# Kernel optimization log

Measured on AMD Instinct MI355X. Metric: run time of the kernel, lower is better.

The kernel has to match this reference:

```python
import jax, jax.numpy as jnp
import numpy as np

B, N1, N2, D, H = 2, 1024, 1024, 2048, 16
DH = D // H  # 128


def _rope_tables(S, d):
    inv = 1.0 / (10000.0 ** (np.arange(0, d, 2, dtype=np.float32) / d))
    ang = np.outer(np.arange(S, dtype=np.float32), inv)  # [S, d/2]
    cos = np.repeat(np.cos(ang), 2, axis=-1).astype(np.float32)  # [S, d] interleaved pairs
    sin = np.repeat(np.sin(ang), 2, axis=-1).astype(np.float32)
    return jnp.asarray(cos), jnp.asarray(sin)


def setup_inputs() -> dict:
    key = jax.random.key(0)
    ks = jax.random.split(key, 24)
    sc = 0.02
    cos1, sin1 = _rope_tables(N1, DH)
    cos2, sin2 = _rope_tables(N2, DH)
    inp = {
        'x_1': jax.random.normal(ks[0], (B, N1, D), dtype=jnp.float32),
        'x_2': jax.random.normal(ks[1], (B, N2, D), dtype=jnp.float32),
        'cos1': cos1, 'sin1': sin1, 'cos2': cos2, 'sin2': sin2,
    }
    names = ['wq1', 'wk1', 'wv1', 'wo1', 'wq2', 'wk2', 'wv2', 'wo2']
    for i, n in enumerate(names):
        inp[n] = jax.random.normal(ks[2 + i], (D, D), dtype=jnp.float32) * sc
        inp['b' + n[1:]] = jax.random.normal(ks[10 + i], (D,), dtype=jnp.float32) * sc
    return inp


def _apply_rope(x, cos, sin):
    # x: [B, H, S, DH]; interleaved-pair rotation (use_real_unbind_dim=-1)
    xr = x.reshape(*x.shape[:-1], -1, 2)
    x_real, x_imag = xr[..., 0], xr[..., 1]
    x_rot = jnp.stack([-x_imag, x_real], axis=-1).reshape(x.shape)
    return x * cos[None, None] + x_rot * sin[None, None]


def _split_heads(t):
    b, n, _ = t.shape
    return t.reshape(b, n, H, DH).transpose(0, 2, 1, 3)  # b h n c


def reference(x_1, x_2, cos1, sin1, cos2, sin2,
              wq1, bq1, wk1, bk1, wv1, bv1, wo1, bo1,
              wq2, bq2, wk2, bk2, wv2, bv2, wo2, bo2):
    len_1 = x_1.shape[1]
    q = jnp.concatenate([x_1 @ wq1 + bq1, x_2 @ wq2 + bq2], axis=1)
    k = jnp.concatenate([x_1 @ wk1 + bk1, x_2 @ wk2 + bk2], axis=1)
    v = jnp.concatenate([x_1 @ wv1 + bv1, x_2 @ wv2 + bv2], axis=1)
    q, k, v = _split_heads(q), _split_heads(k), _split_heads(v)
    q = q * (DH ** -0.5)
    # per-position RoPE on the concatenated stream == per-stream RoPE then concat
    cos = jnp.concatenate([cos1, cos2], axis=0)
    sin = jnp.concatenate([sin1, sin2], axis=0)
    q = _apply_rope(q, cos, sin)
    k = _apply_rope(k, cos, sin)
    # joint attention over both streams (independent/cross_only flags = False)
    scores = jnp.einsum('bhqd,bhkd->bhqk', q, k)
    attn = jax.nn.softmax(scores, axis=-1)
    o = jnp.einsum('bhqk,bhkd->bhqd', attn, v)
    o = o.transpose(0, 2, 1, 3).reshape(o.shape[0], -1, H * DH)  # b n (h c)
    o1 = o[:, :len_1] @ wo1 + bo1
    o2 = o[:, len_1:] @ wo2 + bo2
    return (o1, o2)
```

## Files before the change

kernel.cpp:

```cpp
#include <hip/hip_runtime.h>
#include <hip/hip_bf16.h>

typedef __attribute__((ext_vector_type(4))) float f32x4;
typedef __attribute__((ext_vector_type(8))) short short8;
typedef __attribute__((ext_vector_type(4))) unsigned short us4;
typedef __attribute__((ext_vector_type(2))) unsigned short us2;
typedef unsigned short u16;

__device__ __forceinline__ float bf2f(u16 u) {
  unsigned int x = ((unsigned int)u) << 16;
  float f; __builtin_memcpy(&f, &x, 4); return f;
}
__device__ __forceinline__ u16 f2bf(float f) {
  __hip_bfloat16 h = __float2bfloat16(f);
  u16 u; __builtin_memcpy(&u, &h, 2); return u;
}

#define GLL16(g, l) __builtin_amdgcn_global_load_lds( \
    (const __attribute__((address_space(1))) unsigned int*)(g), \
    (__attribute__((address_space(3))) unsigned int*)(l), 16, 0, 0)

#define MFMA16x32(a, b, c) __builtin_amdgcn_mfma_f32_16x16x32_bf16(a, b, c, 0, 0, 0)


__global__ __launch_bounds__(256) void k_convert_x(const float* __restrict__ x1,
                                                   const float* __restrict__ x2,
                                                   u16* __restrict__ xc) {
  int tid = blockIdx.x * 256 + threadIdx.x;
  int e = tid * 8;
  int m = e >> 11, d = e & 2047;
  int b = m >> 11, n = m & 2047;
  const float* src = (n < 1024) ? (x1 + ((b << 10) + n) * 2048 + d)
                                : (x2 + ((b << 10) + n - 1024) * 2048 + d);
  float4 v0 = *(const float4*)src;
  float4 v1 = *(const float4*)(src + 4);
  us4 a = {f2bf(v0.x), f2bf(v0.y), f2bf(v0.z), f2bf(v0.w)};
  us4 c = {f2bf(v1.x), f2bf(v1.y), f2bf(v1.z), f2bf(v1.w)};
  *(us4*)(xc + e) = a;
  *(us4*)(xc + e + 4) = c;
}

struct W8 { const float* w[8]; };

__global__ __launch_bounds__(256) void k_wt(W8 p, u16* __restrict__ wtbase) {
  __shared__ u16 lt[64][72];
  const float* W = p.w[blockIdx.z];
  u16* Wt = wtbase + (size_t)blockIdx.z * 4194304u;
  int k0 = blockIdx.x * 64, n0 = blockIdx.y * 64;
  int t = threadIdx.x;
#pragma unroll
  for (int i = 0; i < 4; ++i) {
    int lin = t + i * 256;
    int r = lin >> 4, c4 = (lin & 15) * 4;
    float4 v = *(const float4*)&W[(k0 + r) * 2048 + n0 + c4];
    us4 u = {f2bf(v.x), f2bf(v.y), f2bf(v.z), f2bf(v.w)};
    *(us4*)&lt[r][c4] = u;
  }
  __syncthreads();
#pragma unroll
  for (int i = 0; i < 8; ++i) {
    int lin = t + i * 256;
    int rd = lin >> 5, cs = (lin & 31) * 2;
    us2 u = {lt[cs][rd], lt[cs + 1][rd]};
    *(us2*)&Wt[(n0 + rd) * 2048 + k0 + cs] = u;
  }
}

__global__ __launch_bounds__(256) void k_vt(const u16* __restrict__ V, u16* __restrict__ Vt) {
  __shared__ u16 lt[64][72];
  int b = blockIdx.z;
  int s0 = blockIdx.x * 64, d0 = blockIdx.y * 64;
  int t = threadIdx.x;
#pragma unroll
  for (int i = 0; i < 2; ++i) {
    int lin = t + i * 256;
    int r = lin >> 3, c8 = (lin & 7) * 8;
    short8 v = *(const short8*)&V[(b * 2048 + s0 + r) * 2048 + d0 + c8];
    *(short8*)&lt[r][c8] = v;
  }
  __syncthreads();
#pragma unroll
  for (int i = 0; i < 8; ++i) {
    int lin = t + i * 256;
    int rd = lin >> 5, cs = (lin & 31) * 2;
    us2 u = {lt[cs][rd], lt[cs + 1][rd]};
    *(us2*)&Vt[(b * 2048 + d0 + rd) * 2048 + s0 + cs] = u;
  }
}

__global__ __launch_bounds__(256) void k_rope(u16* __restrict__ Qb, u16* __restrict__ Kb,
                                              const float* __restrict__ cos1,
                                              const float* __restrict__ sin1,
                                              const float* __restrict__ cos2,
                                              const float* __restrict__ sin2) {
  u16* T = blockIdx.y ? Kb : Qb;
  const float scale = blockIdx.y ? 1.f : 0.08838834764831843f;
  int tid = blockIdx.x * 256 + threadIdx.x;
  int e = tid * 8;
  int m = e >> 11;
  int n = m & 2047;
  int dh0 = e & 127;
  const float* cr; const float* sr;
  if (n < 1024) { cr = cos1 + n * 128; sr = sin1 + n * 128; }
  else          { cr = cos2 + (n - 1024) * 128; sr = sin2 + (n - 1024) * 128; }
  float4 c0 = *(const float4*)(cr + dh0), c1 = *(const float4*)(cr + dh0 + 4);
  float4 s0 = *(const float4*)(sr + dh0), s1 = *(const float4*)(sr + dh0 + 4);
  short8 xv = *(short8*)(T + e);
  float x0 = bf2f((u16)xv[0]), x1 = bf2f((u16)xv[1]), x2 = bf2f((u16)xv[2]), x3 = bf2f((u16)xv[3]);
  float x4 = bf2f((u16)xv[4]), x5 = bf2f((u16)xv[5]), x6 = bf2f((u16)xv[6]), x7 = bf2f((u16)xv[7]);
  us4 o0 = { f2bf((x0 * c0.x - x1 * s0.x) * scale), f2bf((x1 * c0.x + x0 * s0.x) * scale),
             f2bf((x2 * c0.z - x3 * s0.z) * scale), f2bf((x3 * c0.z + x2 * s0.z) * scale) };
  us4 o1 = { f2bf((x4 * c1.x - x5 * s1.x) * scale), f2bf((x5 * c1.x + x4 * s1.x) * scale),
             f2bf((x6 * c1.z - x7 * s1.z) * scale), f2bf((x7 * c1.z + x6 * s1.z) * scale) };
  *(us4*)(T + e) = o0;
  *(us4*)(T + e + 4) = o1;
}

__device__ __forceinline__ void gemm256_core(const u16* __restrict__ A,
                                             const u16* __restrict__ Bt,
                                             int m0, int nb,
                                             u16* lA, u16* lB,
                                             f32x4 acc[8][4]) {
  const int t = threadIdx.x;
  const int lane = t & 63, wid = t >> 6;
  const int lq = lane & 15, lg = lane >> 4;
  const int wr = wid >> 2, wc = wid & 3;
  const int swz = (lq & 7) << 4;

  u16* lA0 = lA;  u16* lA1 = lA + 256 * 64;
  u16* lB0 = lB;  u16* lB1 = lB + 256 * 64;

  short8 af[4][2];
  short8 bf[2][2][2];

  auto stage = [&](const u16* G, int grow0, u16* lbase, int h, int kt) {
    const int k0 = (kt & 31) * 64;
#pragma unroll
    for (int j = 0; j < 2; ++j) {
      int c = j * 512 + t;
      int row = c >> 3;
      int colb = (c & 7) * 16;
      int sc = colb ^ ((row & 7) << 4);
      GLL16(G + (size_t)(grow0 + h * 128 + row) * 2048 + k0 + (sc >> 1),
            (u16*)((char*)lbase + (h * 128 + row) * 128 + colb));
    }
  };
  auto rdA = [&](const u16* lbase, int mh) {
#pragma unroll
    for (int mf = 0; mf < 4; ++mf)
#pragma unroll
      for (int kc = 0; kc < 2; ++kc) {
        int row = wr * 128 + (mh * 4 + mf) * 16 + lq;
        af[mf][kc] = *(const short8*)((const char*)lbase + row * 128 +
                                      ((kc * 64 + lg * 16) ^ swz));
      }
  };
  auto rdB = [&](const u16* lbase, int nh) {
#pragma unroll
    for (int nf = 0; nf < 2; ++nf)
#pragma unroll
      for (int kc = 0; kc < 2; ++kc) {
        int row = wc * 64 + (nh * 2 + nf) * 16 + lq;
        bf[nh][nf][kc] = *(const short8*)((const char*)lbase + row * 128 +
                                          ((kc * 64 + lg * 16) ^ swz));
      }
  };
  auto mm = [&](int mh, int nh) {
    __builtin_amdgcn_s_setprio(1);
#pragma unroll
    for (int mf = 0; mf < 4; ++mf)
#pragma unroll
      for (int nf = 0; nf < 2; ++nf)
#pragma unroll
        for (int kc = 0; kc < 2; ++kc)
          acc[mh * 4 + mf][nh * 2 + nf] =
              MFMA16x32(af[mf][kc], bf[nh][nf][kc], acc[mh * 4 + mf][nh * 2 + nf]);
    __builtin_amdgcn_s_setprio(0);
    __builtin_amdgcn_sched_barrier(0);
  };

#define LGK0() do { asm volatile("s_waitcnt lgkmcnt(0)" ::: "memory"); \
                    __builtin_amdgcn_sched_barrier(0); } while (0)
#define BAR()  __builtin_amdgcn_s_barrier()
#define VM4()  asm volatile("s_waitcnt vmcnt(4)" ::: "memory")

  stage(Bt, nb, lB0, 0, 0);
  stage(A,  m0, lA0, 0, 0);
  stage(Bt, nb, lB0, 1, 0);
  stage(A,  m0, lA0, 1, 0);
  stage(Bt, nb, lB1, 0, 1);
  stage(A,  m0, lA1, 0, 1);
  VM4();
  BAR();

#pragma unroll 1
  for (int i = 0; i < 16; ++i) {
    const int o1 = 2 * i + 1, e2 = 2 * i + 2, o3 = 2 * i + 3;
    rdA(lA0, 0); rdB(lB0, 0);
    stage(Bt, nb, lB1, 1, o1);
    BAR(); LGK0(); mm(0, 0); BAR();
    rdB(lB0, 1);
    stage(A, m0, lA1, 1, o1);
    BAR(); LGK0(); mm(0, 1); BAR();
    rdA(lA0, 1);
    stage(Bt, nb, lB0, 0, e2);
    BAR(); LGK0(); mm(1, 0); BAR();
    stage(A, m0, lA0, 0, e2);
    BAR(); LGK0(); mm(1, 1);
    VM4(); BAR();
    rdA(lA1, 0); rdB(lB1, 0);
    stage(Bt, nb, lB0, 1, e2);
    BAR(); LGK0(); mm(0, 0); BAR();
    rdB(lB1, 1);
    stage(A, m0, lA0, 1, e2);
    BAR(); LGK0(); mm(0, 1); BAR();
    rdA(lA1, 1);
    stage(Bt, nb, lB1, 0, o3);
    BAR(); LGK0(); mm(1, 0); BAR();
    stage(A, m0, lA1, 0, o3);
    BAR(); LGK0(); mm(1, 1);
    VM4(); BAR();
  }
#undef LGK0
#undef BAR
#undef VM4
}

struct QKV8P {
  const u16* wt[6];
  const float* bias[6];
  u16* out[3];
  const u16* xc;
};

__global__ __launch_bounds__(512, 2) void k_gemm_qkv(QKV8P p) {
  __shared__ __align__(16) u16 lA[2 * 256 * 64];
  __shared__ __align__(16) u16 lB[2 * 256 * 64];
  const int id = blockIdx.x;
  const int xcd = id & 7, sub = id >> 3;
  const int nt = xcd * 3 + (sub >> 4);
  const int mt = sub & 15;
  const int m0 = mt * 256;
  const int type = nt >> 3;
  const int colw = (nt & 7) * 256;
  const int strm = (mt >> 2) & 1;
  const int widx = type * 2 + strm;
  f32x4 acc[8][4];
  const f32x4 z4 = {0.f, 0.f, 0.f, 0.f};
#pragma unroll
  for (int a = 0; a < 8; ++a)
#pragma unroll
    for (int b = 0; b < 4; ++b) acc[a][b] = z4;
  gemm256_core(p.xc, p.wt[widx], m0, colw, lA, lB, acc);
  const int lane = threadIdx.x & 63, wid = threadIdx.x >> 6;
  const int lq = lane & 15, lg = lane >> 4;
  const int wr = wid >> 2, wc = wid & 3;
  u16* out = p.out[type];
  const float* bias = p.bias[widx];
#pragma unroll
  for (int nf = 0; nf < 4; ++nf) {
    int col = colw + wc * 64 + nf * 16 + lq;
    float bv = bias[col];
#pragma unroll
    for (int mf = 0; mf < 8; ++mf) {
      int row0 = m0 + wr * 128 + mf * 16 + lg * 4;
#pragma unroll
      for (int j = 0; j < 4; ++j)
        out[(size_t)(row0 + j) * 2048 + col] = f2bf(acc[mf][nf][j] + bv);
    }
  }
}

__global__ __launch_bounds__(512, 2) void k_gemm_out(const u16* __restrict__ O,
                                                     const u16* __restrict__ wt0,
                                                     const u16* __restrict__ wt1,
                                                     const float* __restrict__ b0,
                                                     const float* __restrict__ b1,
                                                     float* __restrict__ out) {
  __shared__ __align__(16) u16 lA[2 * 256 * 64];
  __shared__ __align__(16) u16 lB[2 * 256 * 64];
  const int id = blockIdx.x;
  const int nt = id & 7, mt = id >> 3;
  const int m0 = mt * 256;
  const int strm = (mt >> 2) & 1;
  f32x4 acc[8][4];
  const f32x4 z4 = {0.f, 0.f, 0.f, 0.f};
#pragma unroll
  for (int a = 0; a < 8; ++a)
#pragma unroll
    for (int b = 0; b < 4; ++b) acc[a][b] = z4;
  gemm256_core(O, strm ? wt1 : wt0, m0, nt * 256, lA, lB, acc);
  const float* bias = strm ? b1 : b0;
  float* obase = strm ? out + 4194304 : out;
  const int lane = threadIdx.x & 63, wid = threadIdx.x >> 6;
  const int lq = lane & 15, lg = lane >> 4;
  const int wr = wid >> 2, wc = wid & 3;
#pragma unroll
  for (int nf = 0; nf < 4; ++nf) {
    int col = nt * 256 + wc * 64 + nf * 16 + lq;
    float bv = bias[col];
#pragma unroll
    for (int mf = 0; mf < 8; ++mf) {
      int row0 = m0 + wr * 128 + mf * 16 + lg * 4;
#pragma unroll
      for (int j = 0; j < 4; ++j) {
        int row = row0 + j;
        int b = row >> 11, n = row & 2047;
        obase[(size_t)(b * 1024 + n - strm * 1024) * 2048 + col] = acc[mf][nf][j] + bv;
      }
    }
  }
}

__global__ __launch_bounds__(256) void k_attn(const u16* __restrict__ Q,
                                              const u16* __restrict__ K,
                                              const u16* __restrict__ Vt,
                                              u16* __restrict__ O) {
  __shared__ __align__(16) u16 kbuf[2][64 * 128];
  __shared__ __align__(16) u16 vbuf[2][128 * 64];
  __shared__ __align__(16) u16 pbuf[4][16 * 88];
  const int t = threadIdx.x, lane = t & 63, w = t >> 6;
  const int lq = lane & 15, g = lane >> 4;
  const int id = blockIdx.x;
  const int lgid = (id & 7) * 64 + (id >> 3);
  const int bh = lgid >> 4, qt = lgid & 15;
  const int b = bh >> 4, h = bh & 15;

  short8 qf[2][4];
#pragma unroll
  for (int u = 0; u < 2; ++u) {
    const u16* Qp = Q + (size_t)(b * 2048 + qt * 128 + w * 32 + u * 16 + lq) * 2048
                    + h * 128 + g * 8;
#pragma unroll
    for (int c = 0; c < 4; ++c) qf[u][c] = *(const short8*)(Qp + c * 32);
  }

  f32x4 oacc[2][8];
  const f32x4 z4 = {0.f, 0.f, 0.f, 0.f};
#pragma unroll
  for (int u = 0; u < 2; ++u)
#pragma unroll
    for (int dc = 0; dc < 8; ++dc) oacc[u][dc] = z4;
  float m_run[2] = {-1e30f, -1e30f}, l_run[2] = {0.f, 0.f};

  const int swz = (lq & 7) << 4;

  auto STAGE = [&](int bs, int kt) {
#pragma unroll
    for (int ii = 0; ii < 4; ++ii) {
      int i = w * 4 + ii;
      int o = i * 1024 + lane * 16;
      {
        int row = o >> 8, colb = o & 255;
        int sc = colb ^ ((row & 7) << 4);
        GLL16(K + (size_t)(b * 2048 + kt + row) * 2048 + h * 128 + (sc >> 1),
              (u16*)((char*)kbuf[bs] + o));
      }
      {
        int row = o >> 7, colb = o & 127;
        int sc = colb ^ ((row & 7) << 4);
        GLL16(Vt + (size_t)(b * 2048 + h * 128 + row) * 2048 + kt + (sc >> 1),
              (u16*)((char*)vbuf[bs] + o));
      }
    }
  };

  STAGE(0, 0);
  asm volatile("s_waitcnt vmcnt(0)" ::: "memory");
  __syncthreads();

  for (int tt = 0; tt < 32; ++tt) {
    const int cb = tt & 1;
    if (tt < 31) STAGE(cb ^ 1, (tt + 1) * 64);

    const char* kb = (const char*)kbuf[cb];
    const char* vb = (const char*)vbuf[cb];
    f32x4 s[2][4];
#pragma unroll
    for (int u = 0; u < 2; ++u)
#pragma unroll
      for (int kg = 0; kg < 4; ++kg) s[u][kg] = z4;
#pragma unroll
    for (int c = 0; c < 4; ++c) {
#pragma unroll
      for (int kg = 0; kg < 4; ++kg) {
        short8 kf = *(const short8*)(kb + (kg * 16 + lq) * 256 + ((c * 64 + g * 16) ^ swz));
        s[0][kg] = MFMA16x32(kf, qf[0][c], s[0][kg]);
        s[1][kg] = MFMA16x32(kf, qf[1][c], s[1][kg]);
      }
    }
    u16* pw = pbuf[w];
    short8 pb[2][2];
#pragma unroll
    for (int u = 0; u < 2; ++u) {
      float pm = -1e30f;
#pragma unroll
      for (int kg = 0; kg < 4; ++kg)
#pragma unroll
        for (int j = 0; j < 4; ++j) pm = fmaxf(pm, s[u][kg][j]);
      pm = fmaxf(pm, __shfl_xor(pm, 16));
      pm = fmaxf(pm, __shfl_xor(pm, 32));
      const float mnew = fmaxf(m_run[u], pm);
      const float r = __expf(m_run[u] - mnew);
      m_run[u] = mnew;
      float ps = 0.f;
#pragma unroll
      for (int kg = 0; kg < 4; ++kg) {
        float p0 = __expf(s[u][kg][0] - mnew), p1 = __expf(s[u][kg][1] - mnew);
        float p2 = __expf(s[u][kg][2] - mnew), p3 = __expf(s[u][kg][3] - mnew);
        ps += (p0 + p1) + (p2 + p3);
        us4 wv = {f2bf(p0), f2bf(p1), f2bf(p2), f2bf(p3)};
        *(us4*)(pw + lq * 88 + kg * 16 + g * 4) = wv;
      }
      ps += __shfl_xor(ps, 16);
      ps += __shfl_xor(ps, 32);
      l_run[u] = l_run[u] * r + ps;
#pragma unroll
      for (int dc = 0; dc < 8; ++dc) oacc[u][dc] = oacc[u][dc] * r;
      pb[u][0] = *(const short8*)(pw + lq * 88 + g * 8);
      pb[u][1] = *(const short8*)(pw + lq * 88 + 32 + g * 8);
    }
#pragma unroll
    for (int kc = 0; kc < 2; ++kc) {
#pragma unroll
      for (int dc = 0; dc < 8; ++dc) {
        short8 vf = *(const short8*)(vb + (dc * 16 + lq) * 128 + ((kc * 64 + g * 16) ^ swz));
        oacc[0][dc] = MFMA16x32(vf, pb[0][kc], oacc[0][dc]);
        oacc[1][dc] = MFMA16x32(vf, pb[1][kc], oacc[1][dc]);
      }
    }
    asm volatile("s_waitcnt vmcnt(0)" ::: "memory");
    __syncthreads();
  }

#pragma unroll
  for (int u = 0; u < 2; ++u) {
    const float inv = 1.f / l_run[u];
    u16* Op = O + (size_t)(b * 2048 + qt * 128 + w * 32 + u * 16 + lq) * 2048
              + h * 128 + g * 4;
#pragma unroll
    for (int dc = 0; dc < 8; ++dc) {
      us4 ov = {f2bf(oacc[u][dc][0] * inv), f2bf(oacc[u][dc][1] * inv),
                f2bf(oacc[u][dc][2] * inv), f2bf(oacc[u][dc][3] * inv)};
      *(us4*)(Op + dc * 16) = ov;
    }
  }
}


extern "C" void kernel_launch(void* const* d_in, const int* in_sizes, int n_in,
                              void* d_out, int out_size, void* d_ws, size_t ws_size,
                              hipStream_t stream) {
  const float* x1   = (const float*)d_in[0];
  const float* x2   = (const float*)d_in[1];
  const float* cos1 = (const float*)d_in[2];
  const float* sin1 = (const float*)d_in[3];
  const float* cos2 = (const float*)d_in[4];
  const float* sin2 = (const float*)d_in[5];
  W8 wp; const float* bias[8];
  for (int i = 0; i < 8; ++i) {
    wp.w[i] = (const float*)d_in[6 + 2 * i];
    bias[i] = (const float*)d_in[7 + 2 * i];
  }
  float* out = (float*)d_out;
  u16* ws = (u16*)d_ws;
  const size_t NX = 8388608;
  const size_t WSZ = 4194304;
  u16* xc = ws;
  u16* wt = ws + NX;
  u16* Qb = wt + 8 * WSZ;
  u16* Kb = Qb + NX;
  u16* Vb = Kb + NX;
  u16* Ob = Vb + NX;
  u16* Vt = xc;
  if (ws_size < (size_t)((Ob + NX) - ws) * sizeof(u16)) return;

  k_convert_x<<<dim3(4096), dim3(256), 0, stream>>>(x1, x2, xc);
  k_wt<<<dim3(32, 32, 8), dim3(256), 0, stream>>>(wp, wt);

  QKV8P qp;
  qp.wt[0] = wt + 0 * WSZ; qp.wt[1] = wt + 4 * WSZ;
  qp.wt[2] = wt + 1 * WSZ; qp.wt[3] = wt + 5 * WSZ;
  qp.wt[4] = wt + 2 * WSZ; qp.wt[5] = wt + 6 * WSZ;
  qp.bias[0] = bias[0]; qp.bias[1] = bias[4];
  qp.bias[2] = bias[1]; qp.bias[3] = bias[5];
  qp.bias[4] = bias[2]; qp.bias[5] = bias[6];
  qp.out[0] = Qb; qp.out[1] = Kb; qp.out[2] = Vb;
  qp.xc = xc;
  k_gemm_qkv<<<dim3(384), dim3(512), 0, stream>>>(qp);

  k_rope<<<dim3(4096, 2), dim3(256), 0, stream>>>(Qb, Kb, cos1, sin1, cos2, sin2);
  k_vt<<<dim3(32, 32, 2), dim3(256), 0, stream>>>(Vb, Vt);
  k_attn<<<dim3(512), dim3(256), 0, stream>>>(Qb, Kb, Vt, Ob);
  k_gemm_out<<<dim3(128), dim3(512), 0, stream>>>(Ob, wt + 3 * WSZ, wt + 7 * WSZ,
                                                  bias[3], bias[7], out);
}
```

Baseline: 387.9 us.

## Double-buffer A fragments and use partial lgkmcnt waits in GEMM core loop

```diff
diff --git a/kernel.cpp b/kernel.cpp
--- a/kernel.cpp
+++ b/kernel.cpp
@@ -116,6 +116,11 @@
   *(us4*)(T + e + 4) = o1;
 }
 
+#define SB()  __builtin_amdgcn_sched_barrier(0)
+#define BAR() __builtin_amdgcn_s_barrier()
+#define VM4() asm volatile("s_waitcnt vmcnt(4)" ::: "memory")
+#define LGKM(n) asm volatile("s_waitcnt lgkmcnt(" #n ")" ::: "memory")
+
 __device__ __forceinline__ void gemm256_core(const u16* __restrict__ A,
                                              const u16* __restrict__ Bt,
                                              int m0, int nb,
@@ -130,7 +135,8 @@
   u16* lA0 = lA;  u16* lA1 = lA + 256 * 64;
   u16* lB0 = lB;  u16* lB1 = lB + 256 * 64;
 
-  short8 af[4][2];
+  short8 afA[4][2];
+  short8 afB[4][2];
   short8 bf[2][2][2];
 
   auto stage = [&](const u16* G, int grow0, u16* lbase, int h, int kt) {
@@ -145,14 +151,14 @@
             (u16*)((char*)lbase + (h * 128 + row) * 128 + colb));
     }
   };
-  auto rdA = [&](const u16* lbase, int mh) {
+  auto rdA = [&](short8 (&dst)[4][2], const u16* lbase, int mh) {
 #pragma unroll
     for (int mf = 0; mf < 4; ++mf)
 #pragma unroll
       for (int kc = 0; kc < 2; ++kc) {
         int row = wr * 128 + (mh * 4 + mf) * 16 + lq;
-        af[mf][kc] = *(const short8*)((const char*)lbase + row * 128 +
-                                      ((kc * 64 + lg * 16) ^ swz));
+        dst[mf][kc] = *(const short8*)((const char*)lbase + row * 128 +
+                                       ((kc * 64 + lg * 16) ^ swz));
       }
   };
   auto rdB = [&](const u16* lbase, int nh) {
@@ -165,7 +171,7 @@
                                           ((kc * 64 + lg * 16) ^ swz));
       }
   };
-  auto mm = [&](int mh, int nh) {
+  auto mmA = [&](int nh) {
     __builtin_amdgcn_s_setprio(1);
 #pragma unroll
     for (int mf = 0; mf < 4; ++mf)
@@ -173,57 +179,59 @@
       for (int nf = 0; nf < 2; ++nf)
 #pragma unroll
         for (int kc = 0; kc < 2; ++kc)
-          acc[mh * 4 + mf][nh * 2 + nf] =
-              MFMA16x32(af[mf][kc], bf[nh][nf][kc], acc[mh * 4 + mf][nh * 2 + nf]);
+          acc[mf][nh * 2 + nf] = MFMA16x32(afA[mf][kc], bf[nh][nf][kc], acc[mf][nh * 2 + nf]);
     __builtin_amdgcn_s_setprio(0);
-    __builtin_amdgcn_sched_barrier(0);
+    SB();
   };
-
-#define LGK0() do { asm volatile("s_waitcnt lgkmcnt(0)" ::: "memory"); \
-                    __builtin_amdgcn_sched_barrier(0); } while (0)
-#define BAR()  __builtin_amdgcn_s_barrier()
-#define VM4()  asm volatile("s_waitcnt vmcnt(4)" ::: "memory")
-
-  stage(Bt, nb, lB0, 0, 0);
-  stage(A,  m0, lA0, 0, 0);
-  stage(Bt, nb, lB0, 1, 0);
-  stage(A,  m0, lA0, 1, 0);
-  stage(Bt, nb, lB1, 0, 1);
-  stage(A,  m0, lA1, 0, 1);
+  auto mmB = [&](int nh) {
+    __builtin_amdgcn_s_setprio(1);
+#pragma unroll
+    for (int mf = 0; mf < 4; ++mf)
+#pragma unroll
+      for (int nf = 0; nf < 2; ++nf)
+#pragma unroll
+        for (int kc = 0; kc < 2; ++kc)
+          acc[4 + mf][nh * 2 + nf] = MFMA16x32(afB[mf][kc], bf[nh][nf][kc], acc[4 + mf][nh * 2 + nf]);
+    __builtin_amdgcn_s_setprio(0);
+    SB();
+  };
+
+  stage(Bt, nb, lB0, 0, 0); stage(A, m0, lA0, 0, 0);
+  stage(Bt, nb, lB0, 1, 0); stage(A, m0, lA0, 1, 0);
+  stage(Bt, nb, lB1, 0, 1); stage(A, m0, lA1, 0, 1);
   VM4();
-  BAR();
+  SB(); BAR();
+  rdA(afA, lA0, 0); rdB(lB0, 0);
 
 #pragma unroll 1
   for (int i = 0; i < 16; ++i) {
     const int o1 = 2 * i + 1, e2 = 2 * i + 2, o3 = 2 * i + 3;
-    rdA(lA0, 0); rdB(lB0, 0);
+    rdB(lB0, 1);
     stage(Bt, nb, lB1, 1, o1);
-    BAR(); LGK0(); mm(0, 0); BAR();
-    rdB(lB0, 1);
+    SB(); BAR(); LGKM(4); SB(); mmA(0); BAR();
+    rdA(afB, lA0, 1);
     stage(A, m0, lA1, 1, o1);
-    BAR(); LGK0(); mm(0, 1); BAR();
-    rdA(lA0, 1);
+    SB(); BAR(); LGKM(8); SB(); mmA(1); BAR();
     stage(Bt, nb, lB0, 0, e2);
-    BAR(); LGK0(); mm(1, 0); BAR();
+    SB(); BAR(); LGKM(0); SB(); mmB(0); BAR();
     stage(A, m0, lA0, 0, e2);
-    BAR(); LGK0(); mm(1, 1);
-    VM4(); BAR();
-    rdA(lA1, 0); rdB(lB1, 0);
+    VM4(); SB(); BAR();
+    rdA(afA, lA1, 0); rdB(lB1, 0);
+    LGKM(12); SB(); mmB(1); BAR();
+    rdB(lB1, 1);
     stage(Bt, nb, lB0, 1, e2);
-    BAR(); LGK0(); mm(0, 0); BAR();
-    rdB(lB1, 1);
+    SB(); BAR(); LGKM(4); SB(); mmA(0); BAR();
+    rdA(afB, lA1, 1);
     stage(A, m0, lA0, 1, e2);
-    BAR(); LGK0(); mm(0, 1); BAR();
-    rdA(lA1, 1);
+    SB(); BAR(); LGKM(8); SB(); mmA(1); BAR();
     stage(Bt, nb, lB1, 0, o3);
-    BAR(); LGK0(); mm(1, 0); BAR();
+    SB(); BAR(); LGKM(0); SB(); mmB(0); BAR();
     stage(A, m0, lA1, 0, o3);
-    BAR(); LGK0(); mm(1, 1);
-    VM4(); BAR();
-  }
-#undef LGK0
-#undef BAR
-#undef VM4
+    VM4(); SB(); BAR();
+    rdA(afA, lA0, 0); rdB(lB0, 0);
+    LGKM(12); SB(); mmB(1); BAR();
+  }
+  asm volatile("s_waitcnt vmcnt(0) lgkmcnt(0)" ::: "memory");
 }
 
 struct QKV8P {
```

Result: slower. 434.0 us (+11.9%).
